# Performance work log

Hardware: AMD Instinct MI355X
Metric: run time of the kernel (lower is better)

Reference implementation:

```python
import jax, jax.numpy as jnp
import numpy as np

S = 14
B = 2
C = 20
LAMBDA_COORD = 5.0
LAMBDA_NOOBJ = 0.5
BATCH = 4096


def setup_inputs() -> dict:
    key = jax.random.key(0)
    k1, k2, k3 = jax.random.split(key, 3)
    pred = jax.random.uniform(k1, (BATCH, S, S, B * 5 + C), dtype=jnp.float32)
    target = jax.random.uniform(k2, (BATCH, S, S, B * 5 + C), dtype=jnp.float32)
    obj = (jax.random.uniform(k3, (BATCH, S, S), dtype=jnp.float32) < 0.15).astype(jnp.float32)
    target = target.at[..., 4].set(obj)
    target = target.at[..., 9].set(obj)
    return {"pred": pred, "target": target}


def _iou(box1, box2):
    # box1, box2: (..., 4) = [x, y, w, h]; elementwise IoU over leading dims
    b1x1 = box1[..., 0] - box1[..., 2] / 2
    b1y1 = box1[..., 1] - box1[..., 3] / 2
    b1x2 = box1[..., 0] + box1[..., 2] / 2
    b1y2 = box1[..., 1] + box1[..., 3] / 2
    b2x1 = box2[..., 0] - box2[..., 2] / 2
    b2y1 = box2[..., 1] - box2[..., 3] / 2
    b2x2 = box2[..., 0] + box2[..., 2] / 2
    b2y2 = box2[..., 1] + box2[..., 3] / 2
    iw = jnp.clip(jnp.minimum(b1x2, b2x2) - jnp.maximum(b1x1, b2x1), 0)
    ih = jnp.clip(jnp.minimum(b1y2, b2y2) - jnp.maximum(b1y1, b2y1), 0)
    inter = iw * ih
    a1 = (b1x2 - b1x1) * (b1y2 - b1y1)
    a2 = (b2x2 - b2x1) * (b2y2 - b2y1)
    return inter / (a1 + a2 - inter + 1e-6)


def reference(pred, target):
    bs = pred.shape[0]
    tb = target[..., : B * 5].reshape(bs, S, S, B, 5)
    pb = pred[..., : B * 5].reshape(bs, S, S, B, 5)
    tcls = target[..., B * 5 :]
    pcls = pred[..., B * 5 :]

    obj_mask = tb[..., 4] > 0          # (bs,S,S,B)
    has_obj = obj_mask[..., 0]         # (bs,S,S)
    noobj_mask = ~obj_mask

    # no-object confidence loss over every non-obj box slot
    conf_err2 = (pb[..., 4] - tb[..., 4]) ** 2
    noobj_loss = jnp.sum(jnp.where(noobj_mask, conf_err2, 0.0))

    # per-box IoU between i-th pred box and i-th target box in each cell
    ious = _iou(pb[..., :4], tb[..., :4])            # (bs,S,S,B)
    best_idx = jnp.argmax(ious, axis=-1)             # (bs,S,S)
    idx = best_idx[..., None, None]
    p_best = jnp.take_along_axis(pb, idx, axis=3)[..., 0, :]  # (bs,S,S,5)
    t_best = jnp.take_along_axis(tb, idx, axis=3)[..., 0, :]

    m = has_obj                                       # (bs,S,S) bool
    mf = m.astype(pred.dtype)

    xy_loss = jnp.sum(mf[..., None] * (p_best[..., :2] - t_best[..., :2]) ** 2)
    p_wh = jnp.sqrt(jnp.abs(p_best[..., 2:4]) + 1e-6)
    t_wh_safe = jnp.where(m[..., None], t_best[..., 2:4], 1.0)  # avoid sqrt(0) grad NaN
    t_wh = jnp.sqrt(t_wh_safe)
    wh_loss = jnp.sum(mf[..., None] * (p_wh - t_wh) ** 2)
    coord_loss = xy_loss + wh_loss

    obj_loss = jnp.sum(mf * (p_best[..., 4] - t_best[..., 4]) ** 2)

    # non-best box confidence pushed to 0 (B=2: the other slot)
    nonbest_conf = jnp.sum(pb[..., 4], axis=-1) - p_best[..., 4]
    noobj_loss = noobj_loss + LAMBDA_NOOBJ * jnp.sum(mf * nonbest_conf ** 2)

    class_loss = jnp.sum(mf[..., None] * (pcls - tcls) ** 2)

    total = LAMBDA_COORD * coord_loss + obj_loss + LAMBDA_NOOBJ * noobj_loss + class_loss
    return total / bs
```

## Files before the change

### kernel.cpp

```cpp
#include <hip/hip_runtime.h>


#define FEAT 30
#define CELLS 802816
#define TPB 256
#define CPB 256
#define NBLOCKS (CELLS / CPB)
#define F4_PER_TILE (CPB * FEAT / 4)

__device__ __forceinline__ float iou_f(float x1, float y1, float w1, float h1,
                                       float x2, float y2, float w2, float h2) {
    float b1x1 = x1 - 0.5f * w1, b1x2 = x1 + 0.5f * w1;
    float b1y1 = y1 - 0.5f * h1, b1y2 = y1 + 0.5f * h1;
    float b2x1 = x2 - 0.5f * w2, b2x2 = x2 + 0.5f * w2;
    float b2y1 = y2 - 0.5f * h2, b2y2 = y2 + 0.5f * h2;
    float iw = fmaxf(fminf(b1x2, b2x2) - fmaxf(b1x1, b2x1), 0.0f);
    float ih = fmaxf(fminf(b1y2, b2y2) - fmaxf(b1y1, b2y1), 0.0f);
    float inter = iw * ih;
    float a1 = (b1x2 - b1x1) * (b1y2 - b1y1);
    float a2 = (b2x2 - b2x1) * (b2y2 - b2y1);
    return inter / (a1 + a2 - inter + 1e-6f);
}

__global__ __launch_bounds__(TPB) void yolo_main_kernel(
        const float* __restrict__ pred, const float* __restrict__ tgt,
        float* __restrict__ partials) {
    __shared__ float sp[CPB * FEAT];
    __shared__ float st[CPB * FEAT];
    __shared__ float wave_sum[TPB / 64];

    const int tid = threadIdx.x;
    const long long base = (long long)blockIdx.x * (CPB * FEAT);

    const float4* gp = (const float4*)(pred + base);
    const float4* gt = (const float4*)(tgt + base);
    float4* lp = (float4*)sp;
    float4* lt = (float4*)st;
#pragma unroll
    for (int i = 0; i < 7; ++i) {
        lp[tid + i * TPB] = gp[tid + i * TPB];
        lt[tid + i * TPB] = gt[tid + i * TPB];
    }
    if (tid < (F4_PER_TILE - 7 * TPB)) {
        lp[tid + 7 * TPB] = gp[tid + 7 * TPB];
        lt[tid + 7 * TPB] = gt[tid + 7 * TPB];
    }
    __syncthreads();

    float p[FEAT], t[FEAT];
    const float2* pc = (const float2*)(sp + tid * FEAT);
    const float2* tc = (const float2*)(st + tid * FEAT);
#pragma unroll
    for (int i = 0; i < FEAT / 2; ++i) {
        float2 vp = pc[i]; p[2 * i] = vp.x; p[2 * i + 1] = vp.y;
        float2 vt = tc[i]; t[2 * i] = vt.x; t[2 * i + 1] = vt.y;
    }

    const bool obj0 = t[4] > 0.0f;
    const bool obj1 = t[9] > 0.0f;
    const float mf = obj0 ? 1.0f : 0.0f;

    float d0 = p[4] - t[4];
    float d1 = p[9] - t[9];
    float noobj = (obj0 ? 0.0f : d0 * d0) + (obj1 ? 0.0f : d1 * d1);

    float iou0 = iou_f(p[0], p[1], p[2], p[3], t[0], t[1], t[2], t[3]);
    float iou1 = iou_f(p[5], p[6], p[7], p[8], t[5], t[6], t[7], t[8]);
    const bool sel1 = iou1 > iou0;

    float pbx = sel1 ? p[5] : p[0];
    float pby = sel1 ? p[6] : p[1];
    float pbw = sel1 ? p[7] : p[2];
    float pbh = sel1 ? p[8] : p[3];
    float pbc = sel1 ? p[9] : p[4];
    float tbx = sel1 ? t[5] : t[0];
    float tby = sel1 ? t[6] : t[1];
    float tbw = sel1 ? t[7] : t[2];
    float tbh = sel1 ? t[8] : t[3];
    float tbc = sel1 ? t[9] : t[4];

    float dx = pbx - tbx, dy = pby - tby;
    float xy = dx * dx + dy * dy;

    float pw = sqrtf(fabsf(pbw) + 1e-6f);
    float ph = sqrtf(fabsf(pbh) + 1e-6f);
    float tw = sqrtf(obj0 ? tbw : 1.0f);
    float th = sqrtf(obj0 ? tbh : 1.0f);
    float dw = pw - tw, dh = ph - th;
    float wh = dw * dw + dh * dh;

    float dc = pbc - tbc;
    float obj_l = dc * dc;

    float nonbest = (p[4] + p[9]) - pbc;
    noobj += 0.5f * mf * nonbest * nonbest;

    float cls = 0.0f;
#pragma unroll
    for (int k = 10; k < FEAT; ++k) {
        float d = p[k] - t[k];
        cls += d * d;
    }

    float cell = 5.0f * mf * (xy + wh) + mf * obj_l + 0.5f * noobj + mf * cls;

    float v = cell;
#pragma unroll
    for (int off = 32; off > 0; off >>= 1) v += __shfl_down(v, off, 64);
    __syncthreads();
    if ((tid & 63) == 0) wave_sum[tid >> 6] = v;
    __syncthreads();
    if (tid == 0)
        partials[blockIdx.x] = wave_sum[0] + wave_sum[1] + wave_sum[2] + wave_sum[3];
}

__global__ __launch_bounds__(TPB) void yolo_reduce_kernel(
        const float* __restrict__ partials, float* __restrict__ out) {
    __shared__ float wave_sum[TPB / 64];
    const int tid = threadIdx.x;
    float v = 0.0f;
    for (int i = tid; i < NBLOCKS; i += TPB) v += partials[i];
#pragma unroll
    for (int off = 32; off > 0; off >>= 1) v += __shfl_down(v, off, 64);
    if ((tid & 63) == 0) wave_sum[tid >> 6] = v;
    __syncthreads();
    if (tid == 0)
        out[0] = (wave_sum[0] + wave_sum[1] + wave_sum[2] + wave_sum[3]) *
                 (1.0f / 4096.0f);
}

extern "C" void kernel_launch(void* const* d_in, const int* in_sizes, int n_in,
                              void* d_out, int out_size, void* d_ws, size_t ws_size,
                              hipStream_t stream) {
    const float* pred = (const float*)d_in[0];
    const float* tgt  = (const float*)d_in[1];
    float* out = (float*)d_out;
    float* partials = (float*)d_ws;

    yolo_main_kernel<<<NBLOCKS, TPB, 0, stream>>>(pred, tgt, partials);
    yolo_reduce_kernel<<<1, TPB, 0, stream>>>(partials, out);
}
```

Before: 205.6 us.

## Reuse one shared-memory tile for pred and target to raise occupancy

Replaces the two per-block shared tiles with a single buffer. Pred is staged, copied into registers, then target is staged into the same buffer. This roughly halves LDS per block, and launch bounds now request five blocks per CU, so more blocks are resident to hide global-memory latency. In exchange, each block loads its two inputs in sequence with an extra barrier, and class features are read straight from LDS. A redundant barrier before the wave reduction is also removed.

```diff
diff --git a/kernel.cpp b/kernel.cpp
--- a/kernel.cpp
+++ b/kernel.cpp
@@ -6,7 +6,7 @@
 #define TPB 256
 #define CPB 256
 #define NBLOCKS (CELLS / CPB)
-#define F4_PER_TILE (CPB * FEAT / 4)
+#define F4_PER_ARRAY (CPB * FEAT / 4)
 
 __device__ __forceinline__ float iou_f(float x1, float y1, float w1, float h1,
                                        float x2, float y2, float w2, float h2) {
@@ -22,38 +22,54 @@
     return inter / (a1 + a2 - inter + 1e-6f);
 }
 
-__global__ __launch_bounds__(TPB) void yolo_main_kernel(
+__global__ __launch_bounds__(TPB, 5) void yolo_main_kernel(
         const float* __restrict__ pred, const float* __restrict__ tgt,
         float* __restrict__ partials) {
-    __shared__ float sp[CPB * FEAT];
-    __shared__ float st[CPB * FEAT];
+    __shared__ float sb[CPB * FEAT];
     __shared__ float wave_sum[TPB / 64];
 
     const int tid = threadIdx.x;
     const long long base = (long long)blockIdx.x * (CPB * FEAT);
 
-    const float4* gp = (const float4*)(pred + base);
-    const float4* gt = (const float4*)(tgt + base);
-    float4* lp = (float4*)sp;
-    float4* lt = (float4*)st;
+    {
+        const float4* g = (const float4*)(pred + base);
+        float4* l = (float4*)sb;
 #pragma unroll
-    for (int i = 0; i < 7; ++i) {
-        lp[tid + i * TPB] = gp[tid + i * TPB];
-        lt[tid + i * TPB] = gt[tid + i * TPB];
-    }
-    if (tid < (F4_PER_TILE - 7 * TPB)) {
-        lp[tid + 7 * TPB] = gp[tid + 7 * TPB];
-        lt[tid + 7 * TPB] = gt[tid + 7 * TPB];
+        for (int i = 0; i < 7; ++i) l[tid + i * TPB] = g[tid + i * TPB];
+        if (tid < (F4_PER_ARRAY - 7 * TPB))
+            l[tid + 7 * TPB] = g[tid + 7 * TPB];
     }
     __syncthreads();
 
-    float p[FEAT], t[FEAT];
-    const float2* pc = (const float2*)(sp + tid * FEAT);
-    const float2* tc = (const float2*)(st + tid * FEAT);
+    float p[FEAT];
+    {
+        const float2* pc = (const float2*)(sb + tid * FEAT);
 #pragma unroll
-    for (int i = 0; i < FEAT / 2; ++i) {
-        float2 vp = pc[i]; p[2 * i] = vp.x; p[2 * i + 1] = vp.y;
-        float2 vt = tc[i]; t[2 * i] = vt.x; t[2 * i + 1] = vt.y;
+        for (int i = 0; i < FEAT / 2; ++i) {
+            float2 v = pc[i];
+            p[2 * i] = v.x;
+            p[2 * i + 1] = v.y;
+        }
+    }
+    __syncthreads();
+
+    {
+        const float4* g = (const float4*)(tgt + base);
+        float4* l = (float4*)sb;
+#pragma unroll
+        for (int i = 0; i < 7; ++i) l[tid + i * TPB] = g[tid + i * TPB];
+        if (tid < (F4_PER_ARRAY - 7 * TPB))
+            l[tid + 7 * TPB] = g[tid + 7 * TPB];
+    }
+    __syncthreads();
+
+    const float2* tc = (const float2*)(sb + tid * FEAT);
+    float t[10];
+#pragma unroll
+    for (int i = 0; i < 5; ++i) {
+        float2 v = tc[i];
+        t[2 * i] = v.x;
+        t[2 * i + 1] = v.y;
     }
 
     const bool obj0 = t[4] > 0.0f;
@@ -97,9 +113,11 @@
 
     float cls = 0.0f;
 #pragma unroll
-    for (int k = 10; k < FEAT; ++k) {
-        float d = p[k] - t[k];
-        cls += d * d;
+    for (int i = 5; i < FEAT / 2; ++i) {
+        float2 v = tc[i];
+        float da = p[2 * i] - v.x;
+        float db = p[2 * i + 1] - v.y;
+        cls += da * da + db * db;
     }
 
     float cell = 5.0f * mf * (xy + wh) + mf * obj_l + 0.5f * noobj + mf * cls;
@@ -107,7 +125,6 @@
     float v = cell;
 #pragma unroll
     for (int off = 32; off > 0; off >>= 1) v += __shfl_down(v, off, 64);
-    __syncthreads();
     if ((tid & 63) == 0) wave_sum[tid >> 6] = v;
     __syncthreads();
     if (tid == 0)
```

Result: no change. 207.3 us (+0.8%).

## Persistent blocks with double-buffered direct global-to-LDS async loads

Applied to the files above, without the earlier changes.

Replaces the one-tile-per-block grid with 256 persistent blocks, each walking 12-13 tiles. Tiles are staged straight into LDS with global_load_lds and double-buffered, using vmcnt waits and barriers so the next tile's load overlaps the current tile's compute. This removes the register round trip of the old copy and the block launch overhead. In exchange, only 256 blocks with one block per CU limit the memory parallelism in flight, and the hand-written waitcnt counting is fragile.

```diff
diff --git a/kernel.cpp b/kernel.cpp
--- a/kernel.cpp
+++ b/kernel.cpp
@@ -5,8 +5,16 @@
 #define CELLS 802816
 #define TPB 256
 #define CPB 256
-#define NBLOCKS (CELLS / CPB)
-#define F4_PER_TILE (CPB * FEAT / 4)
+#define NTILES (CELLS / CPB)
+#define NBLK 256
+#define F4T (CPB * FEAT / 4)
+
+typedef __attribute__((address_space(1))) const unsigned int gas_u32;
+typedef __attribute__((address_space(3))) unsigned int las_u32;
+
+__device__ __forceinline__ void gld_lds16(const float4* g, float4* l) {
+    __builtin_amdgcn_global_load_lds((gas_u32*)g, (las_u32*)l, 16, 0, 0);
+}
 
 __device__ __forceinline__ float iou_f(float x1, float y1, float w1, float h1,
                                        float x2, float y2, float w2, float h2) {
@@ -22,96 +30,129 @@
     return inter / (a1 + a2 - inter + 1e-6f);
 }
 
-__global__ __launch_bounds__(TPB) void yolo_main_kernel(
+__global__ __launch_bounds__(TPB, 1) void yolo_main_kernel(
         const float* __restrict__ pred, const float* __restrict__ tgt,
         float* __restrict__ partials) {
-    __shared__ float sp[CPB * FEAT];
-    __shared__ float st[CPB * FEAT];
-    __shared__ float wave_sum[TPB / 64];
+    __shared__ float4 bP[2][F4T];
+    __shared__ float4 bT[2][F4T];
+    __shared__ float wave_sum[4];
 
-    const int tid = threadIdx.x;
-    const long long base = (long long)blockIdx.x * (CPB * FEAT);
+    const int tid  = threadIdx.x;
+    const int w    = tid >> 6;
+    const int lane = tid & 63;
+    const int b    = blockIdx.x;
+    const int t0 = b * 12 + (b < 64 ? b : 64);
+    const int nt = (b < 64) ? 13 : 12;
 
-    const float4* gp = (const float4*)(pred + base);
-    const float4* gt = (const float4*)(tgt + base);
-    float4* lp = (float4*)sp;
-    float4* lt = (float4*)st;
+    const float4* pred4 = (const float4*)pred;
+    const float4* tgt4  = (const float4*)tgt;
+
+    auto stage = [&](int k, int pp) {
+        const float4* gp = pred4 + (long long)(t0 + k) * F4T;
+        const float4* gt = tgt4  + (long long)(t0 + k) * F4T;
 #pragma unroll
-    for (int i = 0; i < 7; ++i) {
-        lp[tid + i * TPB] = gp[tid + i * TPB];
-        lt[tid + i * TPB] = gt[tid + i * TPB];
+        for (int s = 0; s < 7; ++s) {
+            const int idx = s * 256 + w * 64;
+            gld_lds16(gp + idx + lane, &bP[pp][idx]);
+            gld_lds16(gt + idx + lane, &bT[pp][idx]);
+        }
+        if (lane < 32) {
+            const int idx = 1792 + w * 32;
+            gld_lds16(gp + idx + lane, &bP[pp][idx]);
+            gld_lds16(gt + idx + lane, &bT[pp][idx]);
+        }
+    };
+
+    stage(0, 0);
+    if (nt > 1) stage(1, 1);
+
+    for (int k = 0; k < nt; ++k) {
+        const int pp = k & 1;
+
+        if (k < nt - 1) asm volatile("s_waitcnt vmcnt(16)" ::: "memory");
+        else            asm volatile("s_waitcnt vmcnt(0)"  ::: "memory");
+        __builtin_amdgcn_sched_barrier(0);
+        __builtin_amdgcn_s_barrier();
+        __builtin_amdgcn_sched_barrier(0);
+
+        const float2* pc = (const float2*)((const float*)bP[pp] + tid * FEAT);
+        const float2* tc = (const float2*)((const float*)bT[pp] + tid * FEAT);
+        float p[FEAT], t[FEAT];
+#pragma unroll
+        for (int i = 0; i < FEAT / 2; ++i) {
+            float2 v = pc[i]; p[2 * i] = v.x; p[2 * i + 1] = v.y;
+        }
+#pragma unroll
+        for (int i = 0; i < FEAT / 2; ++i) {
+            float2 v = tc[i]; t[2 * i] = v.x; t[2 * i + 1] = v.y;
+        }
+        asm volatile("s_waitcnt lgkmcnt(0)" ::: "memory");
+        __builtin_amdgcn_sched_barrier(0);
+        __builtin_amdgcn_s_barrier();
+        __builtin_amdgcn_sched_barrier(0);
+
+        if (k + 2 < nt) stage(k + 2, pp);
+
+        const bool obj0 = t[4] > 0.0f;
+        const bool obj1 = t[9] > 0.0f;
+        const float mf = obj0 ? 1.0f : 0.0f;
+
+        float d0 = p[4] - t[4];
+        float d1 = p[9] - t[9];
+        float noobj = (obj0 ? 0.0f : d0 * d0) + (obj1 ? 0.0f : d1 * d1);
+
+        float iou0 = iou_f(p[0], p[1], p[2], p[3], t[0], t[1], t[2], t[3]);
+        float iou1 = iou_f(p[5], p[6], p[7], p[8], t[5], t[6], t[7], t[8]);
+        const bool sel1 = iou1 > iou0;
+
+        float pbx = sel1 ? p[5] : p[0];
+        float pby = sel1 ? p[6] : p[1];
+        float pbw = sel1 ? p[7] : p[2];
+        float pbh = sel1 ? p[8] : p[3];
+        float pbc = sel1 ? p[9] : p[4];
+        float tbx = sel1 ? t[5] : t[0];
+        float tby = sel1 ? t[6] : t[1];
+        float tbw = sel1 ? t[7] : t[2];
+        float tbh = sel1 ? t[8] : t[3];
+        float tbc = sel1 ? t[9] : t[4];
+
+        float dx = pbx - tbx, dy = pby - tby;
+        float xy = dx * dx + dy * dy;
+
+        float pw = sqrtf(fabsf(pbw) + 1e-6f);
+        float ph = sqrtf(fabsf(pbh) + 1e-6f);
+        float tw = sqrtf(obj0 ? tbw : 1.0f);
+        float th = sqrtf(obj0 ? tbh : 1.0f);
+        float dw = pw - tw, dh = ph - th;
+        float wh = dw * dw + dh * dh;
+
+        float dc = pbc - tbc;
+        float obj_l = dc * dc;
+
+        float nonbest = (p[4] + p[9]) - pbc;
+        noobj += 0.5f * mf * nonbest * nonbest;
+
+        float cls = 0.0f;
+#pragma unroll
+        for (int q = 10; q < FEAT; ++q) {
+            float d = p[q] - t[q];
+            cls += d * d;
+        }
+
+        float cell = 5.0f * mf * (xy + wh) + mf * obj_l + 0.5f * noobj + mf * cls;
+
+        float v = cell;
+#pragma unroll
+        for (int off = 32; off > 0; off >>= 1) v += __shfl_down(v, off, 64);
+        if (lane == 0) wave_sum[w] = v;
+        asm volatile("s_waitcnt lgkmcnt(0)" ::: "memory");
+        __builtin_amdgcn_sched_barrier(0);
+        __builtin_amdgcn_s_barrier();
+        __builtin_amdgcn_sched_barrier(0);
+        if (tid == 0)
+            partials[t0 + k] =
+                wave_sum[0] + wave_sum[1] + wave_sum[2] + wave_sum[3];
     }
-    if (tid < (F4_PER_TILE - 7 * TPB)) {
-        lp[tid + 7 * TPB] = gp[tid + 7 * TPB];
-        lt[tid + 7 * TPB] = gt[tid + 7 * TPB];
-    }
-    __syncthreads();
-
-    float p[FEAT], t[FEAT];
-    const float2* pc = (const float2*)(sp + tid * FEAT);
-    const float2* tc = (const float2*)(st + tid * FEAT);
-#pragma unroll
-    for (int i = 0; i < FEAT / 2; ++i) {
-        float2 vp = pc[i]; p[2 * i] = vp.x; p[2 * i + 1] = vp.y;
-        float2 vt = tc[i]; t[2 * i] = vt.x; t[2 * i + 1] = vt.y;
-    }
-
-    const bool obj0 = t[4] > 0.0f;
-    const bool obj1 = t[9] > 0.0f;
-    const float mf = obj0 ? 1.0f : 0.0f;
-
-    float d0 = p[4] - t[4];
-    float d1 = p[9] - t[9];
-    float noobj = (obj0 ? 0.0f : d0 * d0) + (obj1 ? 0.0f : d1 * d1);
-
-    float iou0 = iou_f(p[0], p[1], p[2], p[3], t[0], t[1], t[2], t[3]);
-    float iou1 = iou_f(p[5], p[6], p[7], p[8], t[5], t[6], t[7], t[8]);
-    const bool sel1 = iou1 > iou0;
-
-    float pbx = sel1 ? p[5] : p[0];
-    float pby = sel1 ? p[6] : p[1];
-    float pbw = sel1 ? p[7] : p[2];
-    float pbh = sel1 ? p[8] : p[3];
-    float pbc = sel1 ? p[9] : p[4];
-    float tbx = sel1 ? t[5] : t[0];
-    float tby = sel1 ? t[6] : t[1];
-    float tbw = sel1 ? t[7] : t[2];
-    float tbh = sel1 ? t[8] : t[3];
-    float tbc = sel1 ? t[9] : t[4];
-
-    float dx = pbx - tbx, dy = pby - tby;
-    float xy = dx * dx + dy * dy;
-
-    float pw = sqrtf(fabsf(pbw) + 1e-6f);
-    float ph = sqrtf(fabsf(pbh) + 1e-6f);
-    float tw = sqrtf(obj0 ? tbw : 1.0f);
-    float th = sqrtf(obj0 ? tbh : 1.0f);
-    float dw = pw - tw, dh = ph - th;
-    float wh = dw * dw + dh * dh;
-
-    float dc = pbc - tbc;
-    float obj_l = dc * dc;
-
-    float nonbest = (p[4] + p[9]) - pbc;
-    noobj += 0.5f * mf * nonbest * nonbest;
-
-    float cls = 0.0f;
-#pragma unroll
-    for (int k = 10; k < FEAT; ++k) {
-        float d = p[k] - t[k];
-        cls += d * d;
-    }
-
-    float cell = 5.0f * mf * (xy + wh) + mf * obj_l + 0.5f * noobj + mf * cls;
-
-    float v = cell;
-#pragma unroll
-    for (int off = 32; off > 0; off >>= 1) v += __shfl_down(v, off, 64);
-    __syncthreads();
-    if ((tid & 63) == 0) wave_sum[tid >> 6] = v;
-    __syncthreads();
-    if (tid == 0)
-        partials[blockIdx.x] = wave_sum[0] + wave_sum[1] + wave_sum[2] + wave_sum[3];
 }
 
 __global__ __launch_bounds__(TPB) void yolo_reduce_kernel(
@@ -119,7 +160,7 @@
     __shared__ float wave_sum[TPB / 64];
     const int tid = threadIdx.x;
     float v = 0.0f;
-    for (int i = tid; i < NBLOCKS; i += TPB) v += partials[i];
+    for (int i = tid; i < NTILES; i += TPB) v += partials[i];
 #pragma unroll
     for (int off = 32; off > 0; off >>= 1) v += __shfl_down(v, off, 64);
     if ((tid & 63) == 0) wave_sum[tid >> 6] = v;
@@ -137,6 +178,6 @@
     float* out = (float*)d_out;
     float* partials = (float*)d_ws;
 
-    yolo_main_kernel<<<NBLOCKS, TPB, 0, stream>>>(pred, tgt, partials);
+    yolo_main_kernel<<<NBLK, TPB, 0, stream>>>(pred, tgt, partials);
     yolo_reduce_kernel<<<1, TPB, 0, stream>>>(partials, out);
 }
```

Result: slower. 214.6 us (+4.4%).
